# Optimization experiments

Measured on AMD Instinct MI355X. Metric: run time of the kernel, lower is better.

The kernel has to match this reference:

```python
import jax, jax.numpy as jnp
import numpy as np

TAU_RANK = 0.5
GAMMA_RANK = 1.0
TAU_GATE = 1.0
LN_EPS = 1e-5


def setup_inputs() -> dict:
    key = jax.random.key(0)
    ks = jax.random.split(key, 8)
    B, L, D, H, V = 8, 2048, 768, 1024, 32000
    ids = jax.random.randint(ks[0], (B, L), 0, V)
    embeddings = jax.random.normal(ks[1], (B, L, D), dtype=jnp.float32)
    attn = (jax.random.uniform(ks[2], (B, L)) < 0.9).astype(jnp.float32)
    rhos = jnp.array([0.1, 0.25, 0.5], dtype=jnp.float32)
    ln_g = jnp.ones((D,), jnp.float32)
    ln_b = jnp.zeros((D,), jnp.float32)
    w1 = jax.random.normal(ks[3], (D, H), dtype=jnp.float32) * 0.02
    b1 = jnp.zeros((H,), jnp.float32)
    w2 = jax.random.normal(ks[4], (H, 1), dtype=jnp.float32) * 0.02
    b2 = jnp.zeros((1,), jnp.float32)
    emb_table = jax.random.normal(ks[5], (V, D), dtype=jnp.float32) * 0.02
    return {"ids": ids, "embeddings": embeddings, "attn": attn, "rhos": rhos,
            "ln_g": ln_g, "ln_b": ln_b, "w1": w1, "b1": b1, "w2": w2, "b2": b2,
            "emb_table": emb_table}


def _selector_mlp(x, ln_g, ln_b, w1, b1, w2, b2):
    mu = x.mean(-1, keepdims=True)
    var = ((x - mu) ** 2).mean(-1, keepdims=True)
    x = (x - mu) / jnp.sqrt(var + LN_EPS) * ln_g + ln_b
    x = jax.nn.gelu(x @ w1 + b1, approximate=False)  # dropout eval = identity
    return (x @ w2 + b2)[..., 0]  # [B, L]


def _pool(emb, attn):
    # masked mean pooling: [.., L, D], [.., L] -> [.., D]
    denom = jnp.maximum(attn.sum(-1, keepdims=True), 1.0)
    return (emb * attn[..., None]).sum(-2) / denom


def _soft_rank(scores, attn, tau, gamma=1.0):
    scores = jnp.where(attn == 0, 0.0, scores)
    denom = jnp.maximum(attn.sum(1, keepdims=True), 1.0)
    mean = (scores * attn).sum(1, keepdims=True) / denom
    var = (((scores - mean) ** 2) * attn).sum(1, keepdims=True) / denom
    s = (scores - mean) / jnp.sqrt(var + 1e-6)
    # diff[b,i,j] = s[b,i] - s[b,j]
    p = jax.nn.sigmoid(-(s[:, :, None] - s[:, None, :]) / tau)
    if gamma != 1.0:
        p = p ** gamma
    p = p * (attn[:, None, :] * attn[:, :, None])
    r = 0.5 + p.sum(2)
    return jnp.where(attn == 0, 1e9, r)


def reference(ids, embeddings, attn, rhos, ln_g, ln_b, w1, b1, w2, b2, emb_table):
    attn_f = attn.astype(jnp.float32)
    emb = embeddings * attn_f[..., None]
    scores = _selector_mlp(emb, ln_g, ln_b, w1, b1, w2, b2)
    scores = jnp.where(attn_f == 0, 0.0, scores)

    full_rep = jax.lax.stop_gradient(_pool(embeddings, attn_f))  # [B, D]
    L_eff = attn_f.sum(1)  # [B]
    ranks = _soft_rank(scores, attn_f, TAU_RANK, GAMMA_RANK)  # [B, L]

    B, L = ids.shape
    R = rhos.shape[0]
    k = jnp.round(rhos[:, None] * L_eff[None]).astype(jnp.int32)  # [R, B]
    k = jnp.where(L_eff[None] > 0, jnp.maximum(k, 1), 0)
    k_f = k.astype(jnp.float32)

    gate_raw = jax.nn.sigmoid((k_f[:, :, None] - ranks[None]) / TAU_GATE) * attn_f[None]
    z = gate_raw / jnp.maximum(gate_raw.sum(-1, keepdims=True), 1e-8)
    z = z * k_f[:, :, None]  # [R, B, L]

    invalid_ranks = jnp.where(attn_f == 0, jnp.inf, ranks)
    # rank position of each token = inverse of the sort permutation
    rank_pos = jnp.argsort(jnp.argsort(invalid_ranks, axis=1), axis=1)  # [B, L]
    g = (rank_pos[None] < k[:, :, None]).astype(jnp.float32)  # hard top-k gate [R, B, L]

    g_st = g + (z - jax.lax.stop_gradient(z))  # straight-through
    effective_attn = attn_f[None] * g_st  # [R, B, L]

    tok = emb_table[ids]  # [B, L, D]; shared across R
    pred_rep = _pool(tok[None], effective_attn)  # [R, B, D]

    eps = 1e-8
    num = (pred_rep * full_rep[None]).sum(-1)
    den = jnp.maximum(jnp.linalg.norm(pred_rep, axis=-1), eps) * \
          jnp.maximum(jnp.linalg.norm(full_rep[None] * jnp.ones_like(pred_rep[..., :1]), axis=-1), eps)
    cos = num / den
    loss = (1.0 - cos).mean()
    return z, g, loss
```

## Files before the change

kernel.cpp:

```cpp
#include <hip/hip_runtime.h>
#include <math.h>

#define NB 8
#define NL 2048
#define ND 768
#define NH 1024
#define NR 3
#define NM (NB*NL)
#define LS 32

typedef _Float16 h16;
typedef __attribute__((ext_vector_type(8))) _Float16 h16x8;
typedef __attribute__((ext_vector_type(4))) float f32x4;

#define ASCALE 4.0f
#define BSCALE 64.0f
#define INV_AB (1.0f/(ASCALE*BSCALE))

enum : int {
  WS_MU     = 0,
  WS_ISTD   = WS_MU + NM,
  WS_SCORES = WS_ISTD + NM,
  WS_RANKS  = WS_SCORES + NM,
  WS_LEFF   = WS_RANKS + NM,
  WS_SMEAN  = WS_LEFF + 8,
  WS_SISTD  = WS_SMEAN + 8,
  WS_KF     = WS_SISTD + 8,
  WS_GDEN   = WS_KF + 24,
  WS_CBP    = WS_GDEN + 24,
  WS_SPART  = WS_CBP + 8*NH,
  WS_FPART  = WS_SPART + 16*NM,
  WS_PPART  = WS_FPART + LS*NB*ND,
  WS_RPART  = WS_PPART + LS*NR*NB*ND,
  WS_POSP   = WS_RPART + 4*NM,
  WS_FULL   = WS_POSP + 4*NM,
  WS_PRED   = WS_FULL + NB*ND,
  WS_BTH    = WS_PRED + NR*NB*ND,
  WS_BTL    = WS_BTH + NH*ND/2,
  WS_END    = WS_BTL + NH*ND/2
};

__device__ __forceinline__ float block_sum256(float v) {
  __shared__ float tmp[4];
  __shared__ float res;
  int lane = threadIdx.x & 63;
  int w = threadIdx.x >> 6;
  #pragma unroll
  for (int o = 32; o > 0; o >>= 1) v += __shfl_down(v, o);
  if (lane == 0) tmp[w] = v;
  __syncthreads();
  if (threadIdx.x == 0) res = tmp[0] + tmp[1] + tmp[2] + tmp[3];
  __syncthreads();
  return res;
}

__device__ __forceinline__ void f16split(float v, h16& hi, h16& lo) {
  hi = (h16)v;
  lo = (h16)(v - (float)hi);
}

__global__ void k_leff(const float* __restrict__ attn, float* __restrict__ ws) {
  int b = blockIdx.x, t = threadIdx.x;
  float s = 0.f;
  for (int l = t; l < NL; l += 256) s += attn[b*NL + l];
  float tot = block_sum256(s);
  if (t == 0) ws[WS_LEFF + b] = tot;
}

__global__ void k_stats(const float* __restrict__ emb, const float* __restrict__ attn,
                        float* __restrict__ ws) {
  int w = threadIdx.x >> 6, l = threadIdx.x & 63;
  int m = blockIdx.x*4 + w;
  const float* x = emb + (size_t)m * ND;
  float a = attn[m];
  float4 v0 = *(const float4*)&x[l*4];
  float4 v1 = *(const float4*)&x[256 + l*4];
  float4 v2 = *(const float4*)&x[512 + l*4];
  float s = v0.x+v0.y+v0.z+v0.w + v1.x+v1.y+v1.z+v1.w + v2.x+v2.y+v2.z+v2.w;
  #pragma unroll
  for (int o = 1; o < 64; o <<= 1) s += __shfl_xor(s, o);
  float mu = a * s / (float)ND;
  float q = 0.f;
  float xs[12] = {v0.x,v0.y,v0.z,v0.w, v1.x,v1.y,v1.z,v1.w, v2.x,v2.y,v2.z,v2.w};
  #pragma unroll
  for (int e = 0; e < 12; ++e) { float d = xs[e]*a - mu; q = fmaf(d, d, q); }
  #pragma unroll
  for (int o = 1; o < 64; o <<= 1) q += __shfl_xor(q, o);
  if (l == 0) {
    ws[WS_MU + m] = mu;
    ws[WS_ISTD + m] = 1.f / sqrtf(q / (float)ND + 1e-5f);
  }
}

__global__ void k_fullpart(const float* __restrict__ emb, const float* __restrict__ attn,
                           float* __restrict__ ws) {
  int b = blockIdx.x, dc = blockIdx.y, ls = blockIdx.z;
  int d = dc*256 + threadIdx.x;
  float acc = 0.f;
  int l0 = ls * (NL/LS);
  for (int l = l0; l < l0 + NL/LS; ++l)
    acc = fmaf(emb[((size_t)(b*NL + l))*ND + d], attn[b*NL + l], acc);
  ws[WS_FPART + ls*(NB*ND) + b*ND + d] = acc;
}

__global__ void k_cb(const float* __restrict__ w1, const float* __restrict__ lnb,
                     float* __restrict__ ws) {
  int n = blockIdx.x*256 + threadIdx.x;
  int j = blockIdx.y;
  float s = 0.f;
  for (int k = j*(ND/8); k < (j+1)*(ND/8); ++k)
    s = fmaf(lnb[k], w1[(size_t)k*NH + n], s);
  ws[WS_CBP + j*NH + n] = s;
}

__global__ void k_splitB(const float* __restrict__ w1, const float* __restrict__ lng,
                         float* __restrict__ ws) {
  __shared__ float tile[32][33];
  int bk = blockIdx.x, bn = blockIdx.y, t = threadIdx.x;
  int i = t >> 5, j = t & 31;
  #pragma unroll
  for (int s = 0; s < 4; ++s)
    tile[i + 8*s][j] = w1[(size_t)(bk*32 + i + 8*s)*NH + bn*32 + j];
  __syncthreads();
  h16* bth = (h16*)(ws + WS_BTH);
  h16* btl = (h16*)(ws + WS_BTL);
  int kl = j;
  float lg = lng[bk*32 + kl] * BSCALE;
  #pragma unroll
  for (int s = 0; s < 4; ++s) {
    int nl = i + 8*s;
    int n = bn*32 + nl, k = bk*32 + kl;
    h16 hi, lo;
    f16split(tile[kl][nl] * lg, hi, lo);
    bth[(size_t)n*ND + k] = hi;
    btl[(size_t)n*ND + k] = lo;
  }
}

__global__ void __launch_bounds__(256) k_gemm(
    const float* __restrict__ emb, const float* __restrict__ attn,
    const float* __restrict__ b1, const float* __restrict__ w2,
    float* __restrict__ ws) {
  __shared__ h16 AsH[128][40], AsL[128][40], BsH[128][40], BsL[128][40];
  int t = threadIdx.x;
  int m0 = blockIdx.x * 128, n0 = blockIdx.y * 128;
  int ar = t >> 1, ak = (t & 1) * 16;
  float isv = ws[WS_ISTD + m0 + ar];
  float pco  = ASCALE * attn[m0 + ar] * isv;
  float mqco = -ASCALE * ws[WS_MU + m0 + ar] * isv;
  int lane = t & 63, w = t >> 6, wm = w >> 1, wn = w & 1;
  int fr = lane & 15, g = lane >> 4;
  f32x4 acc[4][4];
  #pragma unroll
  for (int i = 0; i < 4; ++i)
    #pragma unroll
    for (int j = 0; j < 4; ++j) acc[i][j] = (f32x4){0.f, 0.f, 0.f, 0.f};
  const h16* bth = (const h16*)(ws + WS_BTH);
  const h16* btl = (const h16*)(ws + WS_BTL);

  for (int k0 = 0; k0 < ND; k0 += 32) {
    h16 hs[16], lo[16];
    #pragma unroll
    for (int i = 0; i < 4; ++i) {
      float4 x = *(const float4*)&emb[(size_t)(m0 + ar)*ND + k0 + ak + 4*i];
      float xs[4] = {x.x, x.y, x.z, x.w};
      #pragma unroll
      for (int e = 0; e < 4; ++e)
        f16split(fmaf(xs[e], pco, mqco), hs[4*i+e], lo[4*i+e]);
    }
    h16x8 bh0 = *(const h16x8*)&bth[(size_t)(n0 + ar)*ND + k0 + ak];
    h16x8 bh1 = *(const h16x8*)&bth[(size_t)(n0 + ar)*ND + k0 + ak + 8];
    h16x8 bl0 = *(const h16x8*)&btl[(size_t)(n0 + ar)*ND + k0 + ak];
    h16x8 bl1 = *(const h16x8*)&btl[(size_t)(n0 + ar)*ND + k0 + ak + 8];
    __syncthreads();
    *(h16x8*)&AsH[ar][ak]     = (h16x8){hs[0],hs[1],hs[2],hs[3],hs[4],hs[5],hs[6],hs[7]};
    *(h16x8*)&AsH[ar][ak + 8] = (h16x8){hs[8],hs[9],hs[10],hs[11],hs[12],hs[13],hs[14],hs[15]};
    *(h16x8*)&AsL[ar][ak]     = (h16x8){lo[0],lo[1],lo[2],lo[3],lo[4],lo[5],lo[6],lo[7]};
    *(h16x8*)&AsL[ar][ak + 8] = (h16x8){lo[8],lo[9],lo[10],lo[11],lo[12],lo[13],lo[14],lo[15]};
    *(h16x8*)&BsH[ar][ak]     = bh0;
    *(h16x8*)&BsH[ar][ak + 8] = bh1;
    *(h16x8*)&BsL[ar][ak]     = bl0;
    *(h16x8*)&BsL[ar][ak + 8] = bl1;
    __syncthreads();
    h16x8 ah[4], al[4];
    #pragma unroll
    for (int mi = 0; mi < 4; ++mi) {
      int r = wm*64 + mi*16 + fr;
      ah[mi] = *(const h16x8*)&AsH[r][g*8];
      al[mi] = *(const h16x8*)&AsL[r][g*8];
    }
    #pragma unroll
    for (int ni = 0; ni < 4; ++ni) {
      int c = wn*64 + ni*16 + fr;
      h16x8 bh = *(const h16x8*)&BsH[c][g*8];
      h16x8 bl = *(const h16x8*)&BsL[c][g*8];
      #pragma unroll
      for (int mi = 0; mi < 4; ++mi) {
        acc[mi][ni] = __builtin_amdgcn_mfma_f32_16x16x32_f16(ah[mi], bh, acc[mi][ni], 0, 0, 0);
        acc[mi][ni] = __builtin_amdgcn_mfma_f32_16x16x32_f16(ah[mi], bl, acc[mi][ni], 0, 0, 0);
        acc[mi][ni] = __builtin_amdgcn_mfma_f32_16x16x32_f16(al[mi], bh, acc[mi][ni], 0, 0, 0);
      }
    }
  }
  float b1v[4], w2v[4];
  #pragma unroll
  for (int ni = 0; ni < 4; ++ni) {
    int c = n0 + wn*64 + ni*16 + fr;
    float cb = 0.f;
    #pragma unroll
    for (int j = 0; j < 8; ++j) cb += ws[WS_CBP + j*NH + c];
    b1v[ni] = b1[c] + cb;
    w2v[ni] = w2[c];
  }
  #pragma unroll
  for (int mi = 0; mi < 4; ++mi) {
    #pragma unroll
    for (int q = 0; q < 4; ++q) {
      float p = 0.f;
      #pragma unroll
      for (int ni = 0; ni < 4; ++ni) {
        float h = fmaf(acc[mi][ni][q], INV_AB, b1v[ni]);
        float ge = 0.5f * h * (1.f + erff(h * 0.70710678118654752f));
        p = fmaf(ge, w2v[ni], p);
      }
      p += __shfl_xor(p, 1);
      p += __shfl_xor(p, 2);
      p += __shfl_xor(p, 4);
      p += __shfl_xor(p, 8);
      if (fr == 0)
        ws[WS_SPART + (blockIdx.y*2 + wn)*NM + m0 + wm*64 + mi*16 + 4*g + q] = p;
    }
  }
}

__global__ void k_scorered(float* __restrict__ ws, const float* __restrict__ b2) {
  int i = blockIdx.x*256 + threadIdx.x;
  float s = 0.f;
  #pragma unroll
  for (int j = 0; j < 16; ++j) s += ws[WS_SPART + j*NM + i];
  ws[WS_SCORES + i] = s + b2[0];
}

__global__ void k_scorestats(const float* __restrict__ attn, float* __restrict__ ws) {
  int b = blockIdx.x, t = threadIdx.x;
  float s = 0.f;
  for (int l = t; l < NL; l += 256) s += attn[b*NL + l] * ws[WS_SCORES + b*NL + l];
  float tot = block_sum256(s);
  float le = ws[WS_LEFF + b];
  float mean = tot / fmaxf(le, 1.f);
  float v = 0.f;
  for (int l = t; l < NL; l += 256) {
    float a = attn[b*NL + l];
    float d = ws[WS_SCORES + b*NL + l] - mean;
    v = fmaf(a * d, d, v);
  }
  float var = block_sum256(v) / fmaxf(le, 1.f);
  if (t == 0) { ws[WS_SMEAN + b] = mean; ws[WS_SISTD + b] = 1.f / sqrtf(var + 1e-6f); }
}

__global__ void k_rankpart(const float* __restrict__ attn, float* __restrict__ ws) {
  __shared__ float sCh[512];
  int b = blockIdx.x, c = blockIdx.y, js = blockIdx.z, t = threadIdx.x;
  float mean = ws[WS_SMEAN + b], istd = ws[WS_SISTD + b];
  for (int j = t; j < 512; j += 256) {
    int jj = js*512 + j;
    float a = attn[b*NL + jj];
    sCh[j] = (a != 0.f) ? (ws[WS_SCORES + b*NL + jj] - mean) * istd : -1e30f;
  }
  __syncthreads();
  int i = c*256 + t;
  float ai = attn[b*NL + i];
  float si = (ai != 0.f) ? (ws[WS_SCORES + b*NL + i] - mean) * istd : -1e30f;
  float acc = 0.f;
  #pragma unroll 4
  for (int j = 0; j < 512; ++j) {
    float u = (sCh[j] - si) * 2.0f;
    acc += 1.f / (1.f + __expf(-u));
  }
  ws[WS_RPART + js*NM + b*NL + i] = acc;
}

__global__ void k_rankred(const float* __restrict__ attn, float* __restrict__ ws) {
  int i = blockIdx.x*256 + threadIdx.x;
  float r = 0.5f + ws[WS_RPART + i] + ws[WS_RPART + NM + i]
                 + ws[WS_RPART + 2*NM + i] + ws[WS_RPART + 3*NM + i];
  ws[WS_RANKS + i] = (attn[i] != 0.f) ? r : 1e9f;
}

__global__ void k_gatedenom(const float* __restrict__ attn, const float* __restrict__ rhos,
                            float* __restrict__ ws) {
  int rb = blockIdx.x;
  int r = rb / NB, b = rb % NB;
  int t = threadIdx.x;
  float le = ws[WS_LEFF + b];
  float kf = rintf(rhos[r] * le);
  kf = (le > 0.f) ? fmaxf(kf, 1.f) : 0.f;
  float s = 0.f;
  for (int l = t; l < NL; l += 256) {
    float ri = ws[WS_RANKS + b*NL + l];
    s += attn[b*NL + l] / (1.f + __expf(ri - kf));
  }
  float tot = block_sum256(s);
  if (t == 0) { ws[WS_KF + rb] = kf; ws[WS_GDEN + rb] = fmaxf(tot, 1e-8f); }
}

__global__ void k_pospart(float* __restrict__ ws) {
  __shared__ float rCh[512];
  int b = blockIdx.x, c = blockIdx.y, js = blockIdx.z, t = threadIdx.x;
  for (int j = t; j < 512; j += 256) rCh[j] = ws[WS_RANKS + b*NL + js*512 + j];
  __syncthreads();
  int i = c*256 + t;
  float ri = ws[WS_RANKS + b*NL + i];
  int jbase = js*512;
  int cnt = 0;
  #pragma unroll 4
  for (int j = 0; j < 512; ++j) {
    float rj = rCh[j];
    cnt += (rj < ri) || (rj == ri && (jbase + j) < i);
  }
  ws[WS_POSP + js*NM + b*NL + i] = (float)cnt;
}

__global__ void k_zg(const float* __restrict__ attn, const float* __restrict__ ws,
                     float* __restrict__ out) {
  int b = blockIdx.x, c = blockIdx.y, t = threadIdx.x;
  int i = c*256 + t;
  float ri = ws[WS_RANKS + b*NL + i];
  int pos = (int)(ws[WS_POSP + b*NL + i] + ws[WS_POSP + NM + b*NL + i]
                + ws[WS_POSP + 2*NM + b*NL + i] + ws[WS_POSP + 3*NM + b*NL + i]);
  float ai = attn[b*NL + i];
  #pragma unroll
  for (int r = 0; r < NR; ++r) {
    float kf = ws[WS_KF + r*NB + b];
    float gd = ws[WS_GDEN + r*NB + b];
    float gate = ai / (1.f + __expf(ri - kf));
    float z = gate / gd * kf;
    float g = (pos < (int)kf) ? 1.f : 0.f;
    out[((size_t)(r*NB + b))*NL + i] = z;
    out[(size_t)NR*NB*NL + ((size_t)(r*NB + b))*NL + i] = g;
  }
}

__global__ void k_poolpart(const int* __restrict__ ids, const float* __restrict__ tab,
                           const float* __restrict__ out, float* __restrict__ ws) {
  int b = blockIdx.x, dc = blockIdx.y, ls = blockIdx.z;
  int d = dc*256 + threadIdx.x;
  const float* g0 = out + (size_t)NR*NB*NL + ((size_t)(0*NB + b))*NL;
  const float* g1 = out + (size_t)NR*NB*NL + ((size_t)(1*NB + b))*NL;
  const float* g2 = out + (size_t)NR*NB*NL + ((size_t)(2*NB + b))*NL;
  float a0 = 0.f, a1 = 0.f, a2 = 0.f;
  int l0 = ls * (NL/LS);
  for (int l = l0; l < l0 + NL/LS; ++l) {
    float gg0 = g0[l], gg1 = g1[l], gg2 = g2[l];
    if (gg0 + gg1 + gg2 == 0.f) continue;
    float v = tab[(size_t)ids[b*NL + l]*ND + d];
    a0 = fmaf(gg0, v, a0); a1 = fmaf(gg1, v, a1); a2 = fmaf(gg2, v, a2);
  }
  float* pp = ws + WS_PPART + ls*(NR*NB*ND);
  pp[(0*NB + b)*ND + d] = a0;
  pp[(1*NB + b)*ND + d] = a1;
  pp[(2*NB + b)*ND + d] = a2;
}

__global__ void k_prered(float* __restrict__ ws) {
  int idx = blockIdx.x*256 + threadIdx.x;
  if (idx < NB*ND) {
    float s = 0.f;
    #pragma unroll 8
    for (int j = 0; j < LS; ++j) s += ws[WS_FPART + j*(NB*ND) + idx];
    ws[WS_FULL + idx] = s;
  } else {
    int p = idx - NB*ND;
    float s = 0.f;
    #pragma unroll 8
    for (int j = 0; j < LS; ++j) s += ws[WS_PPART + j*(NR*NB*ND) + p];
    ws[WS_PRED + p] = s;
  }
}

__global__ void k_loss(float* __restrict__ ws, float* __restrict__ out) {
  int t = threadIdx.x;
  float lacc = 0.f;
  for (int rb = 0; rb < NR*NB; ++rb) {
    int b = rb % NB;
    float dn = fmaxf(ws[WS_KF + rb], 1.f);
    float le = fmaxf(ws[WS_LEFF + b], 1.f);
    float num = 0.f, p2 = 0.f, f2 = 0.f;
    for (int d = t; d < ND; d += 256) {
      float p = ws[WS_PRED + rb*ND + d] / dn;
      float f = ws[WS_FULL + b*ND + d] / le;
      num = fmaf(p, f, num); p2 = fmaf(p, p, p2); f2 = fmaf(f, f, f2);
    }
    num = block_sum256(num);
    p2 = block_sum256(p2);
    f2 = block_sum256(f2);
    if (t == 0)
      lacc += 1.f - num / (fmaxf(sqrtf(p2), 1e-8f) * fmaxf(sqrtf(f2), 1e-8f));
  }
  if (t == 0) out[(size_t)2*NR*NB*NL] = lacc / (float)(NR*NB);
}

extern "C" void kernel_launch(void* const* d_in, const int* in_sizes, int n_in,
                              void* d_out, int out_size, void* d_ws, size_t ws_size,
                              hipStream_t stream) {
  const int*   ids  = (const int*)d_in[0];
  const float* emb  = (const float*)d_in[1];
  const float* attn = (const float*)d_in[2];
  const float* rhos = (const float*)d_in[3];
  const float* lng  = (const float*)d_in[4];
  const float* lnb  = (const float*)d_in[5];
  const float* w1   = (const float*)d_in[6];
  const float* b1   = (const float*)d_in[7];
  const float* w2   = (const float*)d_in[8];
  const float* b2   = (const float*)d_in[9];
  const float* tab  = (const float*)d_in[10];
  float* out = (float*)d_out;
  float* ws  = (float*)d_ws;

  k_leff      <<<NB, 256, 0, stream>>>(attn, ws);
  k_stats     <<<NM/4, 256, 0, stream>>>(emb, attn, ws);
  k_fullpart  <<<dim3(NB, 3, LS), 256, 0, stream>>>(emb, attn, ws);
  k_cb        <<<dim3(NH/256, 8), 256, 0, stream>>>(w1, lnb, ws);
  k_splitB    <<<dim3(ND/32, NH/32), 256, 0, stream>>>(w1, lng, ws);
  k_gemm      <<<dim3(NM/128, NH/128), 256, 0, stream>>>(emb, attn, b1, w2, ws);
  k_scorered  <<<NM/256, 256, 0, stream>>>(ws, b2);
  k_scorestats<<<NB, 256, 0, stream>>>(attn, ws);
  k_rankpart  <<<dim3(NB, NL/256, 4), 256, 0, stream>>>(attn, ws);
  k_rankred   <<<NM/256, 256, 0, stream>>>(attn, ws);
  k_gatedenom <<<NR*NB, 256, 0, stream>>>(attn, rhos, ws);
  k_pospart   <<<dim3(NB, NL/256, 4), 256, 0, stream>>>(ws);
  k_zg        <<<dim3(NB, NL/256), 256, 0, stream>>>(attn, ws, out);
  k_poolpart  <<<dim3(NB, 3, LS), 256, 0, stream>>>(ids, tab, out, ws);
  k_prered    <<<(NB*ND + NR*NB*ND)/256, 256, 0, stream>>>(ws);
  k_loss      <<<1, 256, 0, stream>>>(ws, out);
}
```

Before: 470.0 us.

## Fuse small reduction kernels, pack f16 splits, and use exp2 sigmoid

Cuts the launch count by folding several small kernels into their neighbours. The lnb·w1 bias is computed inside the weight-split kernel, score reduction and L_eff go into the score-stats kernel, the rank reduction is recomputed where it is consumed, and the pre-reduction plus loss become a per-(r,b) parallel kernel with a tiny final sum. The GEMM A-operand hi/lo split uses packed cvt_pkrtz conversions, and the LDS row padding shrinks from 40 to 36 halves. The sigmoid in the O(L^2) rank loop is rewritten with exp2 and a hardware reciprocal, with scaling pre-folded. Risks include round-toward-zero conversion slightly changing the f16 split, possible LDS bank conflicts with the new padding, and redundant RPART reads.

New measurement: 452.7 us. 3.7% less time.

```diff
diff --git a/kernel.cpp b/kernel.cpp
--- a/kernel.cpp
+++ b/kernel.cpp
@@ -8,8 +8,11 @@
 #define NR 3
 #define NM (NB*NL)
 #define LS 32
+#define LOG2E  1.4426950408889634f
+#define LOG2E2 2.8853900817779268f
 
 typedef _Float16 h16;
+typedef __attribute__((ext_vector_type(2))) _Float16 h16x2;
 typedef __attribute__((ext_vector_type(8))) _Float16 h16x8;
 typedef __attribute__((ext_vector_type(4))) float f32x4;
 
@@ -18,24 +21,22 @@
 #define INV_AB (1.0f/(ASCALE*BSCALE))
 
 enum : int {
-  WS_MU     = 0,
+  WS_SCORES = 0,
+  WS_MU     = WS_SCORES + NM,
   WS_ISTD   = WS_MU + NM,
-  WS_SCORES = WS_ISTD + NM,
-  WS_RANKS  = WS_SCORES + NM,
-  WS_LEFF   = WS_RANKS + NM,
+  WS_LEFF   = WS_ISTD + NM,
   WS_SMEAN  = WS_LEFF + 8,
   WS_SISTD  = WS_SMEAN + 8,
   WS_KF     = WS_SISTD + 8,
   WS_GDEN   = WS_KF + 24,
-  WS_CBP    = WS_GDEN + 24,
-  WS_SPART  = WS_CBP + 8*NH,
+  WS_LOSSP  = WS_GDEN + 24,
+  WS_CBP    = WS_LOSSP + 24,
+  WS_SPART  = WS_CBP + 24*NH,
   WS_FPART  = WS_SPART + 16*NM,
   WS_PPART  = WS_FPART + LS*NB*ND,
   WS_RPART  = WS_PPART + LS*NR*NB*ND,
   WS_POSP   = WS_RPART + 4*NM,
-  WS_FULL   = WS_POSP + 4*NM,
-  WS_PRED   = WS_FULL + NB*ND,
-  WS_BTH    = WS_PRED + NR*NB*ND,
+  WS_BTH    = WS_POSP + 4*NM,
   WS_BTL    = WS_BTH + NH*ND/2,
   WS_END    = WS_BTL + NH*ND/2
 };
@@ -54,17 +55,17 @@
   return res;
 }
 
-__device__ __forceinline__ void f16split(float v, h16& hi, h16& lo) {
-  hi = (h16)v;
-  lo = (h16)(v - (float)hi);
-}
-
-__global__ void k_leff(const float* __restrict__ attn, float* __restrict__ ws) {
-  int b = blockIdx.x, t = threadIdx.x;
-  float s = 0.f;
-  for (int l = t; l < NL; l += 256) s += attn[b*NL + l];
-  float tot = block_sum256(s);
-  if (t == 0) ws[WS_LEFF + b] = tot;
+__device__ __forceinline__ void f16split2(float a, float b, h16x2& hi, h16x2& lo) {
+  auto h = __builtin_amdgcn_cvt_pkrtz(a, b);
+  float ra = a - (float)h[0];
+  float rb = b - (float)h[1];
+  auto l = __builtin_amdgcn_cvt_pkrtz(ra, rb);
+  hi = (h16x2){(h16)h[0], (h16)h[1]};
+  lo = (h16x2){(h16)l[0], (h16)l[1]};
+}
+
+__device__ __forceinline__ float fsig_exp2(float x) {
+  return __builtin_amdgcn_rcpf(1.f + exp2f(x));
 }
 
 __global__ void k_stats(const float* __restrict__ emb, const float* __restrict__ attn,
@@ -103,18 +104,8 @@
   ws[WS_FPART + ls*(NB*ND) + b*ND + d] = acc;
 }
 
-__global__ void k_cb(const float* __restrict__ w1, const float* __restrict__ lnb,
-                     float* __restrict__ ws) {
-  int n = blockIdx.x*256 + threadIdx.x;
-  int j = blockIdx.y;
-  float s = 0.f;
-  for (int k = j*(ND/8); k < (j+1)*(ND/8); ++k)
-    s = fmaf(lnb[k], w1[(size_t)k*NH + n], s);
-  ws[WS_CBP + j*NH + n] = s;
-}
-
-__global__ void k_splitB(const float* __restrict__ w1, const float* __restrict__ lng,
-                         float* __restrict__ ws) {
+__global__ void k_splitBcb(const float* __restrict__ w1, const float* __restrict__ lng,
+                           const float* __restrict__ lnb, float* __restrict__ ws) {
   __shared__ float tile[32][33];
   int bk = blockIdx.x, bn = blockIdx.y, t = threadIdx.x;
   int i = t >> 5, j = t & 31;
@@ -130,10 +121,17 @@
   for (int s = 0; s < 4; ++s) {
     int nl = i + 8*s;
     int n = bn*32 + nl, k = bk*32 + kl;
-    h16 hi, lo;
-    f16split(tile[kl][nl] * lg, hi, lo);
+    float v = tile[kl][nl] * lg;
+    h16 hi = (h16)v;
     bth[(size_t)n*ND + k] = hi;
-    btl[(size_t)n*ND + k] = lo;
+    btl[(size_t)n*ND + k] = (h16)(v - (float)hi);
+  }
+  if (t < 32) {
+    float s = 0.f;
+    #pragma unroll
+    for (int kl2 = 0; kl2 < 32; ++kl2)
+      s = fmaf(lnb[bk*32 + kl2], tile[kl2][t], s);
+    ws[WS_CBP + bk*NH + bn*32 + t] = s;
   }
 }
 
@@ -141,7 +139,7 @@
     const float* __restrict__ emb, const float* __restrict__ attn,
     const float* __restrict__ b1, const float* __restrict__ w2,
     float* __restrict__ ws) {
-  __shared__ h16 AsH[128][40], AsL[128][40], BsH[128][40], BsL[128][40];
+  __shared__ h16 AsH[128][36], AsL[128][36], BsH[128][36], BsL[128][36];
   int t = threadIdx.x;
   int m0 = blockIdx.x * 128, n0 = blockIdx.y * 128;
   int ar = t >> 1, ak = (t & 1) * 16;
@@ -161,22 +159,28 @@
   for (int k0 = 0; k0 < ND; k0 += 32) {
     h16 hs[16], lo[16];
     #pragma unroll
-    for (int i = 0; i < 4; ++i) {
-      float4 x = *(const float4*)&emb[(size_t)(m0 + ar)*ND + k0 + ak + 4*i];
-      float xs[4] = {x.x, x.y, x.z, x.w};
-      #pragma unroll
-      for (int e = 0; e < 4; ++e)
-        f16split(fmaf(xs[e], pco, mqco), hs[4*i+e], lo[4*i+e]);
+    for (int i = 0; i < 2; ++i) {
+      float4 x0 = *(const float4*)&emb[(size_t)(m0 + ar)*ND + k0 + ak + 8*i];
+      float4 x1 = *(const float4*)&emb[(size_t)(m0 + ar)*ND + k0 + ak + 8*i + 4];
+      h16x2 h0, l0v, h1, l1, h2, l2, h3, l3;
+      f16split2(fmaf(x0.x, pco, mqco), fmaf(x0.y, pco, mqco), h0, l0v);
+      f16split2(fmaf(x0.z, pco, mqco), fmaf(x0.w, pco, mqco), h1, l1);
+      f16split2(fmaf(x1.x, pco, mqco), fmaf(x1.y, pco, mqco), h2, l2);
+      f16split2(fmaf(x1.z, pco, mqco), fmaf(x1.w, pco, mqco), h3, l3);
+      hs[8*i+0]=h0[0]; hs[8*i+1]=h0[1]; hs[8*i+2]=h1[0]; hs[8*i+3]=h1[1];
+      hs[8*i+4]=h2[0]; hs[8*i+5]=h2[1]; hs[8*i+6]=h3[0]; hs[8*i+7]=h3[1];
+      lo[8*i+0]=l0v[0]; lo[8*i+1]=l0v[1]; lo[8*i+2]=l1[0]; lo[8*i+3]=l1[1];
+      lo[8*i+4]=l2[0]; lo[8*i+5]=l2[1]; lo[8*i+6]=l3[0]; lo[8*i+7]=l3[1];
     }
     h16x8 bh0 = *(const h16x8*)&bth[(size_t)(n0 + ar)*ND + k0 + ak];
     h16x8 bh1 = *(const h16x8*)&bth[(size_t)(n0 + ar)*ND + k0 + ak + 8];
     h16x8 bl0 = *(const h16x8*)&btl[(size_t)(n0 + ar)*ND + k0 + ak];
     h16x8 bl1 = *(const h16x8*)&btl[(size_t)(n0 + ar)*ND + k0 + ak + 8];
     __syncthreads();
-    *(h16x8*)&AsH[ar][ak]     = (h16x8){hs[0],hs[1],hs[2],hs[3],hs[4],hs[5],hs[6],hs[7]};
-    *(h16x8*)&AsH[ar][ak + 8] = (h16x8){hs[8],hs[9],hs[10],hs[11],hs[12],hs[13],hs[14],hs[15]};
-    *(h16x8*)&AsL[ar][ak]     = (h16x8){lo[0],lo[1],lo[2],lo[3],lo[4],lo[5],lo[6],lo[7]};
-    *(h16x8*)&AsL[ar][ak + 8] = (h16x8){lo[8],lo[9],lo[10],lo[11],lo[12],lo[13],lo[14],lo[15]};
+    *(h16x8*)&AsH[ar][ak]     = *(const h16x8*)&hs[0];
+    *(h16x8*)&AsH[ar][ak + 8] = *(const h16x8*)&hs[8];
+    *(h16x8*)&AsL[ar][ak]     = *(const h16x8*)&lo[0];
+    *(h16x8*)&AsL[ar][ak + 8] = *(const h16x8*)&lo[8];
     *(h16x8*)&BsH[ar][ak]     = bh0;
     *(h16x8*)&BsH[ar][ak + 8] = bh1;
     *(h16x8*)&BsL[ar][ak]     = bl0;
@@ -208,7 +212,7 @@
     int c = n0 + wn*64 + ni*16 + fr;
     float cb = 0.f;
     #pragma unroll
-    for (int j = 0; j < 8; ++j) cb += ws[WS_CBP + j*NH + c];
+    for (int j = 0; j < 24; ++j) cb += ws[WS_CBP + j*NH + c];
     b1v[ni] = b1[c] + cb;
     w2v[ni] = w2[c];
   }
@@ -233,58 +237,56 @@
   }
 }
 
-__global__ void k_scorered(float* __restrict__ ws, const float* __restrict__ b2) {
-  int i = blockIdx.x*256 + threadIdx.x;
-  float s = 0.f;
-  #pragma unroll
-  for (int j = 0; j < 16; ++j) s += ws[WS_SPART + j*NM + i];
-  ws[WS_SCORES + i] = s + b2[0];
-}
-
-__global__ void k_scorestats(const float* __restrict__ attn, float* __restrict__ ws) {
+__global__ void k_scorestats(const float* __restrict__ attn, const float* __restrict__ b2,
+                             float* __restrict__ ws) {
+  __shared__ float sS[NL];
+  __shared__ float aS[NL];
   int b = blockIdx.x, t = threadIdx.x;
-  float s = 0.f;
-  for (int l = t; l < NL; l += 256) s += attn[b*NL + l] * ws[WS_SCORES + b*NL + l];
-  float tot = block_sum256(s);
-  float le = ws[WS_LEFF + b];
-  float mean = tot / fmaxf(le, 1.f);
+  float b2v = b2[0];
+  float sa = 0.f, at = 0.f;
+  for (int l = t; l < NL; l += 256) {
+    float s = 0.f;
+    #pragma unroll
+    for (int j = 0; j < 16; ++j) s += ws[WS_SPART + j*NM + b*NL + l];
+    s += b2v;
+    ws[WS_SCORES + b*NL + l] = s;
+    float a = attn[b*NL + l];
+    sS[l] = s; aS[l] = a;
+    at += a; sa = fmaf(a, s, sa);
+  }
+  float leff = block_sum256(at);
+  float mean = block_sum256(sa) / fmaxf(leff, 1.f);
   float v = 0.f;
   for (int l = t; l < NL; l += 256) {
-    float a = attn[b*NL + l];
-    float d = ws[WS_SCORES + b*NL + l] - mean;
-    v = fmaf(a * d, d, v);
-  }
-  float var = block_sum256(v) / fmaxf(le, 1.f);
-  if (t == 0) { ws[WS_SMEAN + b] = mean; ws[WS_SISTD + b] = 1.f / sqrtf(var + 1e-6f); }
+    float d = sS[l] - mean;
+    v = fmaf(aS[l] * d, d, v);
+  }
+  float var = block_sum256(v) / fmaxf(leff, 1.f);
+  if (t == 0) {
+    ws[WS_LEFF + b] = leff;
+    ws[WS_SMEAN + b] = mean;
+    ws[WS_SISTD + b] = 1.f / sqrtf(var + 1e-6f);
+  }
 }
 
 __global__ void k_rankpart(const float* __restrict__ attn, float* __restrict__ ws) {
   __shared__ float sCh[512];
   int b = blockIdx.x, c = blockIdx.y, js = blockIdx.z, t = threadIdx.x;
-  float mean = ws[WS_SMEAN + b], istd = ws[WS_SISTD + b];
+  float mean = ws[WS_SMEAN + b], istd = ws[WS_SISTD + b] * LOG2E2;
   for (int j = t; j < 512; j += 256) {
     int jj = js*512 + j;
     float a = attn[b*NL + jj];
-    sCh[j] = (a != 0.f) ? (ws[WS_SCORES + b*NL + jj] - mean) * istd : -1e30f;
+    sCh[j] = (a != 0.f) ? (ws[WS_SCORES + b*NL + jj] - mean) * istd : -2.9e30f;
   }
   __syncthreads();
   int i = c*256 + t;
   float ai = attn[b*NL + i];
-  float si = (ai != 0.f) ? (ws[WS_SCORES + b*NL + i] - mean) * istd : -1e30f;
+  float zi = (ai != 0.f) ? (ws[WS_SCORES + b*NL + i] - mean) * istd : -2.9e30f;
   float acc = 0.f;
   #pragma unroll 4
-  for (int j = 0; j < 512; ++j) {
-    float u = (sCh[j] - si) * 2.0f;
-    acc += 1.f / (1.f + __expf(-u));
-  }
+  for (int j = 0; j < 512; ++j)
+    acc += fsig_exp2(zi - sCh[j]);
   ws[WS_RPART + js*NM + b*NL + i] = acc;
-}
-
-__global__ void k_rankred(const float* __restrict__ attn, float* __restrict__ ws) {
-  int i = blockIdx.x*256 + threadIdx.x;
-  float r = 0.5f + ws[WS_RPART + i] + ws[WS_RPART + NM + i]
-                 + ws[WS_RPART + 2*NM + i] + ws[WS_RPART + 3*NM + i];
-  ws[WS_RANKS + i] = (attn[i] != 0.f) ? r : 1e9f;
 }
 
 __global__ void k_gatedenom(const float* __restrict__ attn, const float* __restrict__ rhos,
@@ -297,20 +299,29 @@
   kf = (le > 0.f) ? fmaxf(kf, 1.f) : 0.f;
   float s = 0.f;
   for (int l = t; l < NL; l += 256) {
-    float ri = ws[WS_RANKS + b*NL + l];
-    s += attn[b*NL + l] / (1.f + __expf(ri - kf));
+    int i = b*NL + l;
+    float ri = 0.5f + ws[WS_RPART + i] + ws[WS_RPART + NM + i]
+                    + ws[WS_RPART + 2*NM + i] + ws[WS_RPART + 3*NM + i];
+    s += attn[i] * fsig_exp2((ri - kf) * LOG2E);
   }
   float tot = block_sum256(s);
   if (t == 0) { ws[WS_KF + rb] = kf; ws[WS_GDEN + rb] = fmaxf(tot, 1e-8f); }
 }
 
-__global__ void k_pospart(float* __restrict__ ws) {
+__global__ void k_pospart(const float* __restrict__ attn, float* __restrict__ ws) {
   __shared__ float rCh[512];
   int b = blockIdx.x, c = blockIdx.y, js = blockIdx.z, t = threadIdx.x;
-  for (int j = t; j < 512; j += 256) rCh[j] = ws[WS_RANKS + b*NL + js*512 + j];
+  for (int j = t; j < 512; j += 256) {
+    int jj = b*NL + js*512 + j;
+    float rr = 0.5f + ws[WS_RPART + jj] + ws[WS_RPART + NM + jj]
+                    + ws[WS_RPART + 2*NM + jj] + ws[WS_RPART + 3*NM + jj];
+    rCh[j] = (attn[jj] != 0.f) ? rr : 1e9f;
+  }
   __syncthreads();
-  int i = c*256 + t;
-  float ri = ws[WS_RANKS + b*NL + i];
+  int i = c*256 + t, ii = b*NL + i;
+  float ri = 0.5f + ws[WS_RPART + ii] + ws[WS_RPART + NM + ii]
+                  + ws[WS_RPART + 2*NM + ii] + ws[WS_RPART + 3*NM + ii];
+  ri = (attn[ii] != 0.f) ? ri : 1e9f;
   int jbase = js*512;
   int cnt = 0;
   #pragma unroll 4
@@ -318,22 +329,24 @@
     float rj = rCh[j];
     cnt += (rj < ri) || (rj == ri && (jbase + j) < i);
   }
-  ws[WS_POSP + js*NM + b*NL + i] = (float)cnt;
+  ws[WS_POSP + js*NM + ii] = (float)cnt;
 }
 
 __global__ void k_zg(const float* __restrict__ attn, const float* __restrict__ ws,
                      float* __restrict__ out) {
   int b = blockIdx.x, c = blockIdx.y, t = threadIdx.x;
-  int i = c*256 + t;
-  float ri = ws[WS_RANKS + b*NL + i];
-  int pos = (int)(ws[WS_POSP + b*NL + i] + ws[WS_POSP + NM + b*NL + i]
-                + ws[WS_POSP + 2*NM + b*NL + i] + ws[WS_POSP + 3*NM + b*NL + i]);
-  float ai = attn[b*NL + i];
+  int i = c*256 + t, ii = b*NL + i;
+  float ai = attn[ii];
+  float ri = 0.5f + ws[WS_RPART + ii] + ws[WS_RPART + NM + ii]
+                  + ws[WS_RPART + 2*NM + ii] + ws[WS_RPART + 3*NM + ii];
+  ri = (ai != 0.f) ? ri : 1e9f;
+  int pos = (int)(ws[WS_POSP + ii] + ws[WS_POSP + NM + ii]
+                + ws[WS_POSP + 2*NM + ii] + ws[WS_POSP + 3*NM + ii]);
   #pragma unroll
   for (int r = 0; r < NR; ++r) {
     float kf = ws[WS_KF + r*NB + b];
     float gd = ws[WS_GDEN + r*NB + b];
-    float gate = ai / (1.f + __expf(ri - kf));
+    float gate = ai * fsig_exp2((ri - kf) * LOG2E);
     float z = gate / gd * kf;
     float g = (pos < (int)kf) ? 1.f : 0.f;
     out[((size_t)(r*NB + b))*NL + i] = z;
@@ -362,42 +375,35 @@
   pp[(2*NB + b)*ND + d] = a2;
 }
 
-__global__ void k_prered(float* __restrict__ ws) {
-  int idx = blockIdx.x*256 + threadIdx.x;
-  if (idx < NB*ND) {
-    float s = 0.f;
+__global__ void k_lossp(float* __restrict__ ws) {
+  int rb = blockIdx.x, t = threadIdx.x;
+  int b = rb & 7;
+  float dn = fmaxf(ws[WS_KF + rb], 1.f);
+  float le = fmaxf(ws[WS_LEFF + b], 1.f);
+  float num = 0.f, p2 = 0.f, f2 = 0.f;
+  for (int d = t; d < ND; d += 256) {
+    float ps = 0.f, fs = 0.f;
     #pragma unroll 8
-    for (int j = 0; j < LS; ++j) s += ws[WS_FPART + j*(NB*ND) + idx];
-    ws[WS_FULL + idx] = s;
-  } else {
-    int p = idx - NB*ND;
-    float s = 0.f;
-    #pragma unroll 8
-    for (int j = 0; j < LS; ++j) s += ws[WS_PPART + j*(NR*NB*ND) + p];
-    ws[WS_PRED + p] = s;
-  }
-}
-
-__global__ void k_loss(float* __restrict__ ws, float* __restrict__ out) {
+    for (int j = 0; j < LS; ++j) {
+      ps += ws[WS_PPART + j*(NR*NB*ND) + rb*ND + d];
+      fs += ws[WS_FPART + j*(NB*ND) + b*ND + d];
+    }
+    float p = ps / dn, f = fs / le;
+    num = fmaf(p, f, num); p2 = fmaf(p, p, p2); f2 = fmaf(f, f, f2);
+  }
+  num = block_sum256(num);
+  p2 = block_sum256(p2);
+  f2 = block_sum256(f2);
+  if (t == 0)
+    ws[WS_LOSSP + rb] = 1.f - num / (fmaxf(sqrtf(p2), 1e-8f) * fmaxf(sqrtf(f2), 1e-8f));
+}
+
+__global__ void k_losssum(const float* __restrict__ ws, float* __restrict__ out) {
   int t = threadIdx.x;
-  float lacc = 0.f;
-  for (int rb = 0; rb < NR*NB; ++rb) {
-    int b = rb % NB;
-    float dn = fmaxf(ws[WS_KF + rb], 1.f);
-    float le = fmaxf(ws[WS_LEFF + b], 1.f);
-    float num = 0.f, p2 = 0.f, f2 = 0.f;
-    for (int d = t; d < ND; d += 256) {
-      float p = ws[WS_PRED + rb*ND + d] / dn;
-      float f = ws[WS_FULL + b*ND + d] / le;
-      num = fmaf(p, f, num); p2 = fmaf(p, p, p2); f2 = fmaf(f, f, f2);
-    }
-    num = block_sum256(num);
-    p2 = block_sum256(p2);
-    f2 = block_sum256(f2);
-    if (t == 0)
-      lacc += 1.f - num / (fmaxf(sqrtf(p2), 1e-8f) * fmaxf(sqrtf(f2), 1e-8f));
-  }
-  if (t == 0) out[(size_t)2*NR*NB*NL] = lacc / (float)(NR*NB);
+  float v = (t < NR*NB) ? ws[WS_LOSSP + t] : 0.f;
+  #pragma unroll
+  for (int o = 32; o > 0; o >>= 1) v += __shfl_down(v, o);
+  if (t == 0) out[(size_t)2*NR*NB*NL] = v / (float)(NR*NB);
 }
 
 extern "C" void kernel_launch(void* const* d_in, const int* in_sizes, int n_in,
@@ -417,20 +423,16 @@
   float* out = (float*)d_out;
   float* ws  = (float*)d_ws;
 
-  k_leff      <<<NB, 256, 0, stream>>>(attn, ws);
   k_stats     <<<NM/4, 256, 0, stream>>>(emb, attn, ws);
   k_fullpart  <<<dim3(NB, 3, LS), 256, 0, stream>>>(emb, attn, ws);
-  k_cb        <<<dim3(NH/256, 8), 256, 0, stream>>>(w1, lnb, ws);
-  k_splitB    <<<dim3(ND/32, NH/32), 256, 0, stream>>>(w1, lng, ws);
+  k_splitBcb  <<<dim3(ND/32, NH/32), 256, 0, stream>>>(w1, lng, lnb, ws);
   k_gemm      <<<dim3(NM/128, NH/128), 256, 0, stream>>>(emb, attn, b1, w2, ws);
-  k_scorered  <<<NM/256, 256, 0, stream>>>(ws, b2);
-  k_scorestats<<<NB, 256, 0, stream>>>(attn, ws);
+  k_scorestats<<<NB, 256, 0, stream>>>(attn, b2, ws);
   k_rankpart  <<<dim3(NB, NL/256, 4), 256, 0, stream>>>(attn, ws);
-  k_rankred   <<<NM/256, 256, 0, stream>>>(attn, ws);
   k_gatedenom <<<NR*NB, 256, 0, stream>>>(attn, rhos, ws);
-  k_pospart   <<<dim3(NB, NL/256, 4), 256, 0, stream>>>(ws);
+  k_pospart   <<<dim3(NB, NL/256, 4), 256, 0, stream>>>(attn, ws);
   k_zg        <<<dim3(NB, NL/256), 256, 0, stream>>>(attn, ws, out);
   k_poolpart  <<<dim3(NB, 3, LS), 256, 0, stream>>>(ids, tab, out, ws);
-  k_prered    <<<(NB*ND + NR*NB*ND)/256, 256, 0, stream>>>(ws);
-  k_loss      <<<1, 256, 0, stream>>>(ws, out);
-}
+  k_lossp     <<<NR*NB, 256, 0, stream>>>(ws);
+  k_losssum   <<<1, 64, 0, stream>>>(ws, out);
+}
```
